# Performance work log

Measured on AMD Instinct MI355X. Metric: run time of the kernel, lower is better.

Reference implementation:

```python
import jax, jax.numpy as jnp
import numpy as np

B_, H_, W_, C_ = 8, 56, 56, 96
D_ = int(C_ * 2.0)          # d_inner = 192
N_ = 16                     # d_state
K_ = 4                      # scan directions
R_ = (C_ + 15) // 16        # dt_rank 'auto' = 6
MLP_H = 4 * C_
EPS = 1e-5


def setup_inputs() -> dict:
    key = jax.random.key(0)
    ks = jax.random.split(key, 16)
    s = 0.02
    rn = lambda k, sh, sc=1.0: jax.random.normal(k, sh, dtype=jnp.float32) * sc
    return dict(
        x=rn(ks[0], (B_, H_, W_, C_)),
        ln1_w=jnp.ones((C_,), jnp.float32), ln1_b=jnp.zeros((C_,), jnp.float32),
        in_proj_w=rn(ks[1], (2 * D_, C_), s),
        conv_w=rn(ks[2], (D_, 1, 3, 3), s), conv_b=jnp.zeros((D_,), jnp.float32),
        x_proj_w=rn(ks[3], (K_, R_ + 2 * N_, D_), s),
        dt_proj_w=rn(ks[4], (K_, D_, R_), s),
        dt_proj_b=rn(ks[5], (K_, D_), 0.1),
        A_logs=jax.random.uniform(ks[6], (K_ * D_, N_), jnp.float32, 0.0, 3.0),
        Ds=jnp.ones((K_ * D_,), jnp.float32),
        out_norm_w=jnp.ones((D_,), jnp.float32), out_norm_b=jnp.zeros((D_,), jnp.float32),
        out_proj_w=rn(ks[7], (C_, D_), s),
        ln2_w=jnp.ones((C_,), jnp.float32), ln2_b=jnp.zeros((C_,), jnp.float32),
        fc1_w=rn(ks[8], (MLP_H, C_), s), fc1_b=jnp.zeros((MLP_H,), jnp.float32),
        fc2_w=rn(ks[9], (C_, MLP_H), s), fc2_b=jnp.zeros((C_,), jnp.float32),
    )


def layer_norm(x, w, b):
    m = x.mean(-1, keepdims=True)
    v = ((x - m) ** 2).mean(-1, keepdims=True)
    return (x - m) / jnp.sqrt(v + EPS) * w + b


def ss2d(x, in_proj_w, conv_w, conv_b, x_proj_w, dt_proj_w, dt_proj_b,
         A_logs, Ds, out_norm_w, out_norm_b, out_proj_w):
    Bn, Hh, Ww, C = x.shape
    L = Hh * Ww
    xz = x @ in_proj_w.T                       # (B,H,W,2D)
    xc, z = jnp.split(xz, 2, axis=-1)
    xc = xc.transpose(0, 3, 1, 2)              # (B,D,H,W)
    xc = jax.lax.conv_general_dilated(xc, conv_w, (1, 1), 'SAME',
                                      feature_group_count=D_)
    xc = jax.nn.silu(xc + conv_b[None, :, None, None])
    # cross-scan: 4 traversal orders, each (B,D,L)
    x0 = xc.reshape(Bn, D_, L)
    x1 = xc.transpose(0, 1, 3, 2).reshape(Bn, D_, L)
    xs = jnp.stack([x0, x1, x0[..., ::-1], x1[..., ::-1]], axis=1)  # (B,K,D,L)
    xdbl = jnp.einsum('bkdl,kcd->bkcl', xs, x_proj_w)
    dts, Bs, Cs = jnp.split(xdbl, [R_, R_ + N_], axis=2)            # (B,K,R,L),(B,K,N,L)x2
    dts = jnp.einsum('bkrl,kdr->bkdl', dts, dt_proj_w)
    dts = jax.nn.softplus(dts + dt_proj_b[None, :, :, None])        # (B,K,D,L)
    A = -jnp.exp(A_logs).reshape(K_, D_, N_)                        # (K,D,N)

    def step(h, inp):
        xt, dtt, Bt, Ct = inp                  # (B,K,D),(B,K,D),(B,K,N),(B,K,N)
        h = h * jnp.exp(dtt[..., None] * A) + (dtt * xt)[..., None] * Bt[:, :, None, :]
        return h, jnp.einsum('bkdn,bkn->bkd', h, Ct)

    inps = (xs.transpose(3, 0, 1, 2), dts.transpose(3, 0, 1, 2),
            Bs.transpose(3, 0, 1, 2), Cs.transpose(3, 0, 1, 2))
    h0 = jnp.zeros((Bn, K_, D_, N_), jnp.float32)
    _, ys = jax.lax.scan(step, h0, inps)       # (L,B,K,D)
    ys = ys.transpose(1, 2, 3, 0)              # (B,K,D,L)
    ys = ys + Ds.reshape(K_, D_)[None, :, :, None] * xs
    # cross-merge: undo flips and transposed order
    y = ys[:, 0] + ys[:, 2, :, ::-1]
    y = y + (ys[:, 1] + ys[:, 3, :, ::-1]).reshape(Bn, D_, Ww, Hh) \
            .transpose(0, 1, 3, 2).reshape(Bn, D_, L)
    y = y.transpose(0, 2, 1).reshape(Bn, Hh, Ww, D_)
    y = layer_norm(y, out_norm_w, out_norm_b)
    y = y * jax.nn.silu(z)
    return y @ out_proj_w.T


def reference(x, ln1_w, ln1_b, in_proj_w, conv_w, conv_b, x_proj_w, dt_proj_w,
              dt_proj_b, A_logs, Ds, out_norm_w, out_norm_b, out_proj_w,
              ln2_w, ln2_b, fc1_w, fc1_b, fc2_w, fc2_b):
    # norm -> SS2D -> residual
    x = x + ss2d(layer_norm(x, ln1_w, ln1_b), in_proj_w, conv_w, conv_b,
                 x_proj_w, dt_proj_w, dt_proj_b, A_logs, Ds,
                 out_norm_w, out_norm_b, out_proj_w)
    # norm -> MLP -> residual
    h = layer_norm(x, ln2_w, ln2_b)
    h = jax.nn.gelu(h @ fc1_w.T + fc1_b) @ fc2_w.T + fc2_b
    return x + h
```

## Files before the change

### kernel.cpp

```cpp
#include <hip/hip_runtime.h>
#include <hip/hip_bf16.h>

typedef __hip_bfloat16 bf16;
typedef short bf16x8 __attribute__((ext_vector_type(8)));
typedef float f32x4 __attribute__((ext_vector_type(4)));

#define BBATCH 8
#define HHH 56
#define WWW 56
#define CCH 96
#define DIN 192
#define NST 16
#define KDIR 4
#define RDT 6
#define LLEN 3136
#define BLTOT 25088
#define SSEG 64
#define SEGL 49
#define PJC 38
#define PJW 152
#define PJS 40
#define PJS1 24
#define MLPH 384

#if defined(__has_builtin)
#if __has_builtin(__builtin_amdgcn_exp2f)
#define EXP2F(x) __builtin_amdgcn_exp2f(x)
#endif
#if __has_builtin(__builtin_amdgcn_logf)
#define LOG2F_(x) __builtin_amdgcn_logf(x)
#endif
#endif
#ifndef EXP2F
#define EXP2F(x) __expf((x) * 0.69314718056f)
#endif
#ifndef LOG2F_
#define LOG2F_(x) (__logf(x) * 1.44269504f)
#endif
#define LOG2E 1.44269504f

__device__ __forceinline__ float b2f(bf16 v) { return __bfloat162float(v); }
__device__ __forceinline__ bf16  f2b(float v) { return __float2bfloat16(v); }
__device__ __forceinline__ unsigned short f2bu(float f) {
    union { bf16 h; unsigned short u; } c; c.h = __float2bfloat16(f); return c.u;
}
__device__ __forceinline__ float sigm(float x) { return 1.f / (1.f + __expf(-x)); }
__device__ __forceinline__ float softplusf(float x) {
    float t = EXP2F(-fabsf(x) * LOG2E);
    return fmaxf(x, 0.f) + 0.69314718f * LOG2F_(1.f + t);
}
__device__ __forceinline__ float geluf(float v) {
    float u = 0.7978845608028654f * (v + 0.044715f * v * v * v);
    float ey = __expf(2.f * u);
    float th = 1.f - 2.f / (ey + 1.f);
    return 0.5f * v * (1.f + th);
}

__device__ __forceinline__ int pos_map(int k, int l) {
    if (k & 2) l = LLEN - 1 - l;
    if (k & 1) { int q = l / WWW; int r = l - q * WWW; return r * WWW + q; }
    return l;
}

__global__ __launch_bounds__(256) void ln_rows(
    const float* __restrict__ xin, const float* __restrict__ w,
    const float* __restrict__ b, unsigned short* __restrict__ xn) {
    int row = blockIdx.x * 4 + (threadIdx.x >> 6);
    int lane = threadIdx.x & 63;
    const float* xr = xin + (size_t)row * 96;
    float2 v = make_float2(0.f, 0.f);
    if (lane < 48) v = *(const float2*)&xr[lane * 2];
    float s = v.x + v.y, s2 = v.x * v.x + v.y * v.y;
    for (int o = 32; o; o >>= 1) {
        s += __shfl_down(s, o);
        s2 += __shfl_down(s2, o);
    }
    s = __shfl(s, 0); s2 = __shfl(s2, 0);
    float m = s * (1.f / 96.f);
    float var = s2 * (1.f / 96.f) - m * m;
    float rs = rsqrtf(var + 1e-5f);
    if (lane < 48) {
        float o0 = (v.x - m) * rs * w[lane * 2] + b[lane * 2];
        float o1 = (v.y - m) * rs * w[lane * 2 + 1] + b[lane * 2 + 1];
        ushort2 u; u.x = f2bu(o0); u.y = f2bu(o1);
        *(ushort2*)&xn[(size_t)row * 96 + lane * 2] = u;
    }
}

template<int N, int K, int EPI>
__global__ __launch_bounds__(256) void gemm_mfma(
    const unsigned short* __restrict__ X, const float* __restrict__ W,
    const float* __restrict__ bias, const float* __restrict__ res,
    void* __restrict__ out0v, void* __restrict__ out1v) {
    __shared__ unsigned short a_sh[256 * 40];
    __shared__ unsigned short b_sh[64 * 40];
    const int t = threadIdx.x;
    const int P0 = blockIdx.x * 256;
    const int N0 = blockIdx.y * 64;
    const int w = t >> 6, lane = t & 63, q = lane >> 4, nl = lane & 15;
    f32x4 acc[4][4];
#pragma unroll
    for (int i = 0; i < 4; ++i)
#pragma unroll
        for (int j = 0; j < 4; ++j)
            acc[i][j] = (f32x4){0.f, 0.f, 0.f, 0.f};
    for (int k0 = 0; k0 < K; k0 += 32) {
        __syncthreads();
#pragma unroll
        for (int it = 0; it < 4; ++it) {
            int idx = t + it * 256;
            int pr = idx >> 2, kq = idx & 3;
            uint4 v = *(const uint4*)&X[(size_t)(P0 + pr) * K + k0 + kq * 8];
            *(uint4*)&a_sh[pr * 40 + kq * 8] = v;
        }
#pragma unroll
        for (int it = 0; it < 2; ++it) {
            int idx = t + it * 256;
            int nr = idx >> 3, kq = idx & 7;
            int ng = N0 + nr; if (ng > N - 1) ng = N - 1;
            float4 v = *(const float4*)&W[(size_t)ng * K + k0 + kq * 4];
            ushort4 u;
            u.x = f2bu(v.x); u.y = f2bu(v.y); u.z = f2bu(v.z); u.w = f2bu(v.w);
            *(ushort4*)&b_sh[nr * 40 + kq * 4] = u;
        }
        __syncthreads();
        bf16x8 af[4], bfr[4];
#pragma unroll
        for (int mf = 0; mf < 4; ++mf)
            af[mf] = *(const bf16x8*)&a_sh[(w * 64 + mf * 16 + nl) * 40 + q * 8];
#pragma unroll
        for (int nf = 0; nf < 4; ++nf)
            bfr[nf] = *(const bf16x8*)&b_sh[(nf * 16 + nl) * 40 + q * 8];
#pragma unroll
        for (int mf = 0; mf < 4; ++mf)
#pragma unroll
            for (int nf = 0; nf < 4; ++nf)
                acc[mf][nf] = __builtin_amdgcn_mfma_f32_16x16x32_bf16(
                    af[mf], bfr[nf], acc[mf][nf], 0, 0, 0);
    }
#pragma unroll
    for (int mf = 0; mf < 4; ++mf) {
#pragma unroll
        for (int nf = 0; nf < 4; ++nf) {
#pragma unroll
            for (int r = 0; r < 4; ++r) {
                float v = acc[mf][nf][r];
                size_t pos = (size_t)P0 + w * 64 + mf * 16 + q * 4 + r;
                int n = N0 + nf * 16 + nl;
                if constexpr (EPI == 0) {
                    unsigned short* xc = (unsigned short*)out0v;
                    unsigned short* zz = (unsigned short*)out1v;
                    if (n < 192) xc[pos * 192 + n] = f2bu(v);
                    else         zz[pos * 192 + (n - 192)] = f2bu(v);
                } else if constexpr (EPI == 1) {
                    if (n < 152) ((float*)out0v)[pos * 152 + n] = v;
                } else if constexpr (EPI == 2) {
                    if (n < 96) ((float*)out0v)[pos * 96 + n] = res[pos * 96 + n] + v;
                } else if constexpr (EPI == 3) {
                    ((unsigned short*)out0v)[pos * 384 + n] = f2bu(geluf(v + bias[n]));
                } else {
                    if (n < 96) ((float*)out0v)[pos * 96 + n] =
                        res[pos * 96 + n] + bias[n] + v;
                }
            }
        }
    }
}

__global__ __launch_bounds__(256) void k2_conv(
    const unsigned short* __restrict__ xcpre, const float* __restrict__ cw,
    const float* __restrict__ cb, unsigned short* __restrict__ xconv) {
    int idx = blockIdx.x * 256 + threadIdx.x;
    int dd = idx % 96;
    int P = idx / 96;
    int d0 = dd * 2;
    int b = P / LLEN, l = P - b * LLEN;
    int h = l / WWW, w = l - h * WWW;
    float acc0 = cb[d0], acc1 = cb[d0 + 1];
#pragma unroll
    for (int i = 0; i < 3; ++i) {
        int hh = h + i - 1;
        if (hh < 0 || hh >= HHH) continue;
#pragma unroll
        for (int j = 0; j < 3; ++j) {
            int ww = w + j - 1;
            if (ww < 0 || ww >= WWW) continue;
            ushort2 xv = *(const ushort2*)&xcpre[
                ((size_t)(b * LLEN + hh * WWW + ww)) * DIN + d0];
            union { unsigned short u; bf16 h_; } c0, c1;
            c0.u = xv.x; c1.u = xv.y;
            acc0 = fmaf(b2f(c0.h_), cw[d0 * 9 + i * 3 + j], acc0);
            acc1 = fmaf(b2f(c1.h_), cw[(d0 + 1) * 9 + i * 3 + j], acc1);
        }
    }
    acc0 = acc0 * sigm(acc0);
    acc1 = acc1 * sigm(acc1);
    ushort2 o; o.x = f2bu(acc0); o.y = f2bu(acc1);
    *(ushort2*)&xconv[(size_t)P * DIN + d0] = o;
}

__global__ __launch_bounds__(192) void k4_scan1(
    const bf16* __restrict__ xconv, const float* __restrict__ proj,
    const float* __restrict__ dtw, const float* __restrict__ dtb,
    const float* __restrict__ Alog, float* __restrict__ hloc,
    float* __restrict__ tsum) {
    __shared__ float pl[SEGL * PJS1];
    __shared__ int posl[SEGL];
    const int bid = blockIdx.x;
    const int s = bid & 63, k = (bid >> 6) & 3, b = bid >> 8;
    const int d = threadIdx.x;
    const int l0 = s * SEGL;
    for (int q = d; q < SEGL * 22; q += 192) {
        int st = q / 22, c = q - st * 22;
        int p = pos_map(k, l0 + st);
        int ofs = (c < 6) ? c : c + 2;
        pl[st * PJS1 + ofs] = proj[(size_t)(b * LLEN + p) * PJW + k * PJC + c];
    }
    if (d < SEGL) posl[d] = pos_map(k, l0 + d) * DIN;
    float w6[RDT];
#pragma unroll
    for (int r = 0; r < RDT; ++r) w6[r] = dtw[(k * DIN + d) * RDT + r];
    const float bias = dtb[k * DIN + d];
    float a2[NST];
#pragma unroll
    for (int n = 0; n < NST; ++n)
        a2[n] = -__expf(Alog[(k * DIN + d) * NST + n]) * LOG2E;
    float h[NST];
#pragma unroll
    for (int n = 0; n < NST; ++n) h[n] = 0.f;
    float T = 0.f;
    __syncthreads();
    const bf16* xg = xconv + (size_t)b * LLEN * DIN + d;
    for (int bt = 0; bt < 7; ++bt) {
        int off7[7]; float xv7[7];
#pragma unroll
        for (int i = 0; i < 7; ++i) off7[i] = posl[bt * 7 + i];
#pragma unroll
        for (int i = 0; i < 7; ++i) xv7[i] = b2f(xg[off7[i]]);
#pragma unroll
        for (int i = 0; i < 7; ++i) {
            const float* rowf = &pl[(bt * 7 + i) * PJS1];
            float4 g0 = *(const float4*)(rowf);
            float2 g1 = *(const float2*)(rowf + 4);
            float dtv = bias;
            dtv = fmaf(g0.x, w6[0], dtv); dtv = fmaf(g0.y, w6[1], dtv);
            dtv = fmaf(g0.z, w6[2], dtv); dtv = fmaf(g0.w, w6[3], dtv);
            dtv = fmaf(g1.x, w6[4], dtv); dtv = fmaf(g1.y, w6[5], dtv);
            dtv = softplusf(dtv);
            T += dtv;
            float u = dtv * xv7[i];
#pragma unroll
            for (int g = 0; g < 4; ++g) {
                float4 Bv = *(const float4*)(rowf + 8 + 4 * g);
                float e0 = EXP2F(dtv * a2[4 * g + 0]);
                float e1 = EXP2F(dtv * a2[4 * g + 1]);
                float e2 = EXP2F(dtv * a2[4 * g + 2]);
                float e3 = EXP2F(dtv * a2[4 * g + 3]);
                h[4 * g + 0] = fmaf(h[4 * g + 0], e0, u * Bv.x);
                h[4 * g + 1] = fmaf(h[4 * g + 1], e1, u * Bv.y);
                h[4 * g + 2] = fmaf(h[4 * g + 2], e2, u * Bv.z);
                h[4 * g + 3] = fmaf(h[4 * g + 3], e3, u * Bv.w);
            }
        }
    }
    size_t base = ((size_t)bid * DIN + d) * NST;
#pragma unroll
    for (int n = 0; n < NST; ++n) hloc[base + n] = h[n];
    tsum[bid * DIN + d] = T;
}

__global__ __launch_bounds__(256) void k5_carry(
    const float* hloc, const float* __restrict__ tsum,
    const float* __restrict__ Alog, float* hin) {
    int g = blockIdx.x * 256 + threadIdx.x;
    int n = g & 15;
    int dk = g >> 4;
    int d = dk % DIN;
    int bk = dk / DIN;
    int k = bk & 3;
    float a2 = -__expf(Alog[(k * DIN + d) * NST + n]) * LOG2E;
    float Hc = 0.f;
    for (int s = 0; s < SSEG; ++s) {
        int bid = bk * SSEG + s;
        size_t idx = ((size_t)bid * DIN + d) * NST + n;
        float hl = hloc[idx];
        float Tv = tsum[bid * DIN + d];
        hin[idx] = Hc;
        Hc = fmaf(EXP2F(a2 * Tv), Hc, hl);
    }
}

__global__ __launch_bounds__(192) void k6_scan2(
    const bf16* __restrict__ xconv, const float* __restrict__ proj,
    const float* __restrict__ dtw, const float* __restrict__ dtb,
    const float* __restrict__ Alog, const float* __restrict__ Dsp,
    const float* __restrict__ hin, bf16* __restrict__ ysm) {
    __shared__ float pl[SEGL * PJS];
    __shared__ int posl[SEGL];
    const int bid = blockIdx.x;
    const int s = bid & 63, k = (bid >> 6) & 3, b = bid >> 8;
    const int d = threadIdx.x;
    const int l0 = s * SEGL;
    for (int q = d; q < SEGL * PJC; q += 192) {
        int st = q / PJC, c = q - st * PJC;
        int p = pos_map(k, l0 + st);
        int ofs = (c < 6) ? c : c + 2;
        pl[st * PJS + ofs] = proj[(size_t)(b * LLEN + p) * PJW + k * PJC + c];
    }
    if (d < SEGL) posl[d] = pos_map(k, l0 + d) * DIN;
    float w6[RDT];
#pragma unroll
    for (int r = 0; r < RDT; ++r) w6[r] = dtw[(k * DIN + d) * RDT + r];
    const float bias = dtb[k * DIN + d];
    const float dsv = Dsp[k * DIN + d];
    float a2[NST];
#pragma unroll
    for (int n = 0; n < NST; ++n)
        a2[n] = -__expf(Alog[(k * DIN + d) * NST + n]) * LOG2E;
    float h[NST];
    size_t hbase = ((size_t)bid * DIN + d) * NST;
#pragma unroll
    for (int n = 0; n < NST; ++n) h[n] = hin[hbase + n];
    __syncthreads();
    const bf16* xg = xconv + (size_t)b * LLEN * DIN + d;
    bf16* ysg = ysm + ((size_t)(b * KDIR + k) * LLEN) * DIN + d;
    for (int bt = 0; bt < 7; ++bt) {
        int off7[7]; float xv7[7];
#pragma unroll
        for (int i = 0; i < 7; ++i) off7[i] = posl[bt * 7 + i];
#pragma unroll
        for (int i = 0; i < 7; ++i) xv7[i] = b2f(xg[off7[i]]);
#pragma unroll
        for (int i = 0; i < 7; ++i) {
            const float* rowf = &pl[(bt * 7 + i) * PJS];
            float4 g0 = *(const float4*)(rowf);
            float2 g1 = *(const float2*)(rowf + 4);
            float dtv = bias;
            dtv = fmaf(g0.x, w6[0], dtv); dtv = fmaf(g0.y, w6[1], dtv);
            dtv = fmaf(g0.z, w6[2], dtv); dtv = fmaf(g0.w, w6[3], dtv);
            dtv = fmaf(g1.x, w6[4], dtv); dtv = fmaf(g1.y, w6[5], dtv);
            dtv = softplusf(dtv);
            float u = dtv * xv7[i];
            float y = dsv * xv7[i];
#pragma unroll
            for (int g = 0; g < 4; ++g) {
                float4 Bv = *(const float4*)(rowf + 8 + 4 * g);
                float4 Cv = *(const float4*)(rowf + 24 + 4 * g);
                float e0 = EXP2F(dtv * a2[4 * g + 0]);
                float e1 = EXP2F(dtv * a2[4 * g + 1]);
                float e2 = EXP2F(dtv * a2[4 * g + 2]);
                float e3 = EXP2F(dtv * a2[4 * g + 3]);
                h[4 * g + 0] = fmaf(h[4 * g + 0], e0, u * Bv.x);
                h[4 * g + 1] = fmaf(h[4 * g + 1], e1, u * Bv.y);
                h[4 * g + 2] = fmaf(h[4 * g + 2], e2, u * Bv.z);
                h[4 * g + 3] = fmaf(h[4 * g + 3], e3, u * Bv.w);
                y = fmaf(h[4 * g + 0], Cv.x, y);
                y = fmaf(h[4 * g + 1], Cv.y, y);
                y = fmaf(h[4 * g + 2], Cv.z, y);
                y = fmaf(h[4 * g + 3], Cv.w, y);
            }
            ysg[off7[i]] = f2b(y);
        }
    }
}

__global__ __launch_bounds__(256) void k65_merge(
    const bf16* __restrict__ ysm, const bf16* __restrict__ z,
    const float* __restrict__ onw, const float* __restrict__ onb,
    bf16* __restrict__ ymod) {
    __shared__ float rb[16 * DIN];
    __shared__ float ps[256], pq[256];
    __shared__ float mrow[16], srow[16];
    const int t = threadIdx.x;
    const int P0 = blockIdx.x * 16;
    for (int q = t; q < 16 * DIN; q += 256) {
        int pos = q / DIN, c = q - pos * DIN;
        int P = P0 + pos;
        int b = P / LLEN, l = P - b * LLEN;
        size_t base = ((size_t)(b * KDIR) * LLEN + l) * DIN + c;
        size_t pstr = (size_t)LLEN * DIN;
        float v = b2f(ysm[base]) + b2f(ysm[base + pstr]) +
                  b2f(ysm[base + 2 * pstr]) + b2f(ysm[base + 3 * pstr]);
        rb[q] = v;
    }
    __syncthreads();
    {
        int pos = t >> 4, part = t & 15;
        float s = 0.f, s2 = 0.f;
        for (int i = 0; i < 12; ++i) {
            float v = rb[pos * DIN + part * 12 + i];
            s += v; s2 += v * v;
        }
        ps[pos * 16 + part] = s; pq[pos * 16 + part] = s2;
    }
    __syncthreads();
    if (t < 16) {
        float s = 0.f, s2 = 0.f;
        for (int i = 0; i < 16; ++i) { s += ps[t * 16 + i]; s2 += pq[t * 16 + i]; }
        float m = s * (1.f / DIN);
        float v = s2 * (1.f / DIN) - m * m;
        mrow[t] = m; srow[t] = rsqrtf(v + 1e-5f);
    }
    __syncthreads();
    for (int q = t; q < 16 * DIN; q += 256) {
        int pos = q / DIN, c = q - pos * DIN;
        int P = P0 + pos;
        float v = (rb[q] - mrow[pos]) * srow[pos] * onw[c] + onb[c];
        float zv = b2f(z[(size_t)P * DIN + c]);
        v *= zv * sigm(zv);
        ymod[(size_t)P * DIN + c] = f2b(v);
    }
}

extern "C" void kernel_launch(void* const* d_in, const int* in_sizes, int n_in,
                              void* d_out, int out_size, void* d_ws, size_t ws_size,
                              hipStream_t stream) {
    const float* x      = (const float*)d_in[0];
    const float* ln1w   = (const float*)d_in[1];
    const float* ln1b   = (const float*)d_in[2];
    const float* inpW   = (const float*)d_in[3];
    const float* convW  = (const float*)d_in[4];
    const float* convB  = (const float*)d_in[5];
    const float* xprojW = (const float*)d_in[6];
    const float* dtW    = (const float*)d_in[7];
    const float* dtB    = (const float*)d_in[8];
    const float* Alog   = (const float*)d_in[9];
    const float* Dsp    = (const float*)d_in[10];
    const float* onw    = (const float*)d_in[11];
    const float* onb    = (const float*)d_in[12];
    const float* outW   = (const float*)d_in[13];
    const float* ln2w   = (const float*)d_in[14];
    const float* ln2b   = (const float*)d_in[15];
    const float* fc1W   = (const float*)d_in[16];
    const float* fc1b   = (const float*)d_in[17];
    const float* fc2W   = (const float*)d_in[18];
    const float* fc2b   = (const float*)d_in[19];
    float* out = (float*)d_out;

    char* ws = (char*)d_ws;
    unsigned short* z_us    = (unsigned short*)(ws + 0);
    bf16*  z_bf             = (bf16*)z_us;
    bf16*  xconv_bf         = (bf16*)(ws + 9633792);
    float* proj_f           = (float*)(ws + 19267584);
    bf16*  ymod_bf          = (bf16*)(ws + 19267584);
    unsigned short* xn_us   = (unsigned short*)(ws + 34521088);
    float* tsum_f           = (float*)(ws + 34521088);
    unsigned short* xcpre_us= (unsigned short*)(ws + 39337984);
    float* hloc_f           = (float*)(ws + 48971776);
    float* hin_f            = hloc_f;
    float* y1_f             = (float*)(ws + 48971776);
    unsigned short* y1n_us  = (unsigned short*)(ws + 58605568);
    bf16*  ysm_bf           = (bf16*)(ws + 74137600);
    unsigned short* hmlp_us = (unsigned short*)(ws + 74137600);

    ln_rows<<<6272, 256, 0, stream>>>(x, ln1w, ln1b, xn_us);
    gemm_mfma<384, 96, 0><<<dim3(98, 6), 256, 0, stream>>>(
        xn_us, inpW, nullptr, nullptr, xcpre_us, z_us);
    k2_conv<<<9408, 256, 0, stream>>>(xcpre_us, convW, convB,
                                      (unsigned short*)xconv_bf);
    gemm_mfma<152, 192, 1><<<dim3(98, 3), 256, 0, stream>>>(
        (const unsigned short*)xconv_bf, xprojW, nullptr, nullptr, proj_f, nullptr);
    k4_scan1<<<2048, 192, 0, stream>>>(xconv_bf, proj_f, dtW, dtB, Alog, hloc_f, tsum_f);
    k5_carry<<<384, 256, 0, stream>>>(hloc_f, tsum_f, Alog, hin_f);
    k6_scan2<<<2048, 192, 0, stream>>>(xconv_bf, proj_f, dtW, dtB, Alog, Dsp, hin_f, ysm_bf);
    k65_merge<<<1568, 256, 0, stream>>>(ysm_bf, z_bf, onw, onb, ymod_bf);
    gemm_mfma<96, 192, 2><<<dim3(98, 2), 256, 0, stream>>>(
        (const unsigned short*)ymod_bf, outW, nullptr, x, y1_f, nullptr);
    ln_rows<<<6272, 256, 0, stream>>>(y1_f, ln2w, ln2b, y1n_us);
    gemm_mfma<384, 96, 3><<<dim3(98, 6), 256, 0, stream>>>(
        y1n_us, fc1W, fc1b, nullptr, hmlp_us, nullptr);
    gemm_mfma<96, 384, 4><<<dim3(98, 2), 256, 0, stream>>>(
        hmlp_us, fc2W, fc2b, y1_f, out, nullptr);
}
```

Baseline: 396.6 us.

## Halve GEMM row tile, widen conv vectors, pack scan math into v_pk_f32

GEMM blocks now cover 128 rows instead of 256, which doubles the grid for better CU occupancy on the small GEMMs. The depthwise conv now handles 4 channels per thread with 8-byte loads, halving its grid. Both scan kernels keep the state and decay terms in float2 pairs and use inline-asm v_pk_mul_f32 and v_pk_fma_f32 to cut VALU instruction count in the recurrence. The y reduction in scan2 is split into two packed partial sums, which changes the summation order slightly. The inline asm may also block some compiler scheduling.

```diff
diff --git a/kernel.cpp b/kernel.cpp
--- a/kernel.cpp
+++ b/kernel.cpp
@@ -39,10 +39,24 @@
 #endif
 #define LOG2E 1.44269504f
 
+__device__ __forceinline__ float2 pk_mul(float2 a, float2 b) {
+    float2 d;
+    asm("v_pk_mul_f32 %0, %1, %2" : "=v"(d) : "v"(a), "v"(b));
+    return d;
+}
+__device__ __forceinline__ float2 pk_fma(float2 a, float2 b, float2 c) {
+    float2 d;
+    asm("v_pk_fma_f32 %0, %1, %2, %3" : "=v"(d) : "v"(a), "v"(b), "v"(c));
+    return d;
+}
+
 __device__ __forceinline__ float b2f(bf16 v) { return __bfloat162float(v); }
 __device__ __forceinline__ bf16  f2b(float v) { return __float2bfloat16(v); }
 __device__ __forceinline__ unsigned short f2bu(float f) {
     union { bf16 h; unsigned short u; } c; c.h = __float2bfloat16(f); return c.u;
+}
+__device__ __forceinline__ float bu2f(unsigned short u) {
+    union { unsigned short u; bf16 h; } c; c.u = u; return __bfloat162float(c.h);
 }
 __device__ __forceinline__ float sigm(float x) { return 1.f / (1.f + __expf(-x)); }
 __device__ __forceinline__ float softplusf(float x) {
@@ -92,22 +106,22 @@
     const unsigned short* __restrict__ X, const float* __restrict__ W,
     const float* __restrict__ bias, const float* __restrict__ res,
     void* __restrict__ out0v, void* __restrict__ out1v) {
-    __shared__ unsigned short a_sh[256 * 40];
+    __shared__ unsigned short a_sh[128 * 40];
     __shared__ unsigned short b_sh[64 * 40];
     const int t = threadIdx.x;
-    const int P0 = blockIdx.x * 256;
+    const int P0 = blockIdx.x * 128;
     const int N0 = blockIdx.y * 64;
     const int w = t >> 6, lane = t & 63, q = lane >> 4, nl = lane & 15;
-    f32x4 acc[4][4];
-#pragma unroll
-    for (int i = 0; i < 4; ++i)
+    f32x4 acc[2][4];
+#pragma unroll
+    for (int i = 0; i < 2; ++i)
 #pragma unroll
         for (int j = 0; j < 4; ++j)
             acc[i][j] = (f32x4){0.f, 0.f, 0.f, 0.f};
     for (int k0 = 0; k0 < K; k0 += 32) {
         __syncthreads();
 #pragma unroll
-        for (int it = 0; it < 4; ++it) {
+        for (int it = 0; it < 2; ++it) {
             int idx = t + it * 256;
             int pr = idx >> 2, kq = idx & 3;
             uint4 v = *(const uint4*)&X[(size_t)(P0 + pr) * K + k0 + kq * 8];
@@ -124,28 +138,28 @@
             *(ushort4*)&b_sh[nr * 40 + kq * 4] = u;
         }
         __syncthreads();
-        bf16x8 af[4], bfr[4];
-#pragma unroll
-        for (int mf = 0; mf < 4; ++mf)
-            af[mf] = *(const bf16x8*)&a_sh[(w * 64 + mf * 16 + nl) * 40 + q * 8];
+        bf16x8 af[2], bfr[4];
+#pragma unroll
+        for (int mf = 0; mf < 2; ++mf)
+            af[mf] = *(const bf16x8*)&a_sh[(w * 32 + mf * 16 + nl) * 40 + q * 8];
 #pragma unroll
         for (int nf = 0; nf < 4; ++nf)
             bfr[nf] = *(const bf16x8*)&b_sh[(nf * 16 + nl) * 40 + q * 8];
 #pragma unroll
-        for (int mf = 0; mf < 4; ++mf)
+        for (int mf = 0; mf < 2; ++mf)
 #pragma unroll
             for (int nf = 0; nf < 4; ++nf)
                 acc[mf][nf] = __builtin_amdgcn_mfma_f32_16x16x32_bf16(
                     af[mf], bfr[nf], acc[mf][nf], 0, 0, 0);
     }
 #pragma unroll
-    for (int mf = 0; mf < 4; ++mf) {
+    for (int mf = 0; mf < 2; ++mf) {
 #pragma unroll
         for (int nf = 0; nf < 4; ++nf) {
 #pragma unroll
             for (int r = 0; r < 4; ++r) {
                 float v = acc[mf][nf][r];
-                size_t pos = (size_t)P0 + w * 64 + mf * 16 + q * 4 + r;
+                size_t pos = (size_t)P0 + w * 32 + mf * 16 + q * 4 + r;
                 int n = N0 + nf * 16 + nl;
                 if constexpr (EPI == 0) {
                     unsigned short* xc = (unsigned short*)out0v;
@@ -171,12 +185,12 @@
     const unsigned short* __restrict__ xcpre, const float* __restrict__ cw,
     const float* __restrict__ cb, unsigned short* __restrict__ xconv) {
     int idx = blockIdx.x * 256 + threadIdx.x;
-    int dd = idx % 96;
-    int P = idx / 96;
-    int d0 = dd * 2;
+    int dd = idx % 48;
+    int P = idx / 48;
+    int d0 = dd * 4;
     int b = P / LLEN, l = P - b * LLEN;
     int h = l / WWW, w = l - h * WWW;
-    float acc0 = cb[d0], acc1 = cb[d0 + 1];
+    float acc0 = cb[d0], acc1 = cb[d0 + 1], acc2 = cb[d0 + 2], acc3 = cb[d0 + 3];
 #pragma unroll
     for (int i = 0; i < 3; ++i) {
         int hh = h + i - 1;
@@ -185,18 +199,19 @@
         for (int j = 0; j < 3; ++j) {
             int ww = w + j - 1;
             if (ww < 0 || ww >= WWW) continue;
-            ushort2 xv = *(const ushort2*)&xcpre[
+            ushort4 xv = *(const ushort4*)&xcpre[
                 ((size_t)(b * LLEN + hh * WWW + ww)) * DIN + d0];
-            union { unsigned short u; bf16 h_; } c0, c1;
-            c0.u = xv.x; c1.u = xv.y;
-            acc0 = fmaf(b2f(c0.h_), cw[d0 * 9 + i * 3 + j], acc0);
-            acc1 = fmaf(b2f(c1.h_), cw[(d0 + 1) * 9 + i * 3 + j], acc1);
-        }
-    }
-    acc0 = acc0 * sigm(acc0);
-    acc1 = acc1 * sigm(acc1);
-    ushort2 o; o.x = f2bu(acc0); o.y = f2bu(acc1);
-    *(ushort2*)&xconv[(size_t)P * DIN + d0] = o;
+            acc0 = fmaf(bu2f(xv.x), cw[(d0 + 0) * 9 + i * 3 + j], acc0);
+            acc1 = fmaf(bu2f(xv.y), cw[(d0 + 1) * 9 + i * 3 + j], acc1);
+            acc2 = fmaf(bu2f(xv.z), cw[(d0 + 2) * 9 + i * 3 + j], acc2);
+            acc3 = fmaf(bu2f(xv.w), cw[(d0 + 3) * 9 + i * 3 + j], acc3);
+        }
+    }
+    acc0 = acc0 * sigm(acc0); acc1 = acc1 * sigm(acc1);
+    acc2 = acc2 * sigm(acc2); acc3 = acc3 * sigm(acc3);
+    ushort4 o;
+    o.x = f2bu(acc0); o.y = f2bu(acc1); o.z = f2bu(acc2); o.w = f2bu(acc3);
+    *(ushort4*)&xconv[(size_t)P * DIN + d0] = o;
 }
 
 __global__ __launch_bounds__(192) void k4_scan1(
@@ -221,13 +236,15 @@
 #pragma unroll
     for (int r = 0; r < RDT; ++r) w6[r] = dtw[(k * DIN + d) * RDT + r];
     const float bias = dtb[k * DIN + d];
-    float a2[NST];
-#pragma unroll
-    for (int n = 0; n < NST; ++n)
-        a2[n] = -__expf(Alog[(k * DIN + d) * NST + n]) * LOG2E;
-    float h[NST];
-#pragma unroll
-    for (int n = 0; n < NST; ++n) h[n] = 0.f;
+    float2 a2[8];
+#pragma unroll
+    for (int j = 0; j < 8; ++j) {
+        a2[j].x = -__expf(Alog[(k * DIN + d) * NST + 2 * j]) * LOG2E;
+        a2[j].y = -__expf(Alog[(k * DIN + d) * NST + 2 * j + 1]) * LOG2E;
+    }
+    float2 h2[8];
+#pragma unroll
+    for (int j = 0; j < 8; ++j) h2[j] = make_float2(0.f, 0.f);
     float T = 0.f;
     __syncthreads();
     const bf16* xg = xconv + (size_t)b * LLEN * DIN + d;
@@ -248,24 +265,26 @@
             dtv = fmaf(g1.x, w6[4], dtv); dtv = fmaf(g1.y, w6[5], dtv);
             dtv = softplusf(dtv);
             T += dtv;
-            float u = dtv * xv7[i];
+            float2 dt2 = make_float2(dtv, dtv);
+            float2 u2 = make_float2(dtv * xv7[i], dtv * xv7[i]);
 #pragma unroll
             for (int g = 0; g < 4; ++g) {
                 float4 Bv = *(const float4*)(rowf + 8 + 4 * g);
-                float e0 = EXP2F(dtv * a2[4 * g + 0]);
-                float e1 = EXP2F(dtv * a2[4 * g + 1]);
-                float e2 = EXP2F(dtv * a2[4 * g + 2]);
-                float e3 = EXP2F(dtv * a2[4 * g + 3]);
-                h[4 * g + 0] = fmaf(h[4 * g + 0], e0, u * Bv.x);
-                h[4 * g + 1] = fmaf(h[4 * g + 1], e1, u * Bv.y);
-                h[4 * g + 2] = fmaf(h[4 * g + 2], e2, u * Bv.z);
-                h[4 * g + 3] = fmaf(h[4 * g + 3], e3, u * Bv.w);
+                float2 Blo = make_float2(Bv.x, Bv.y);
+                float2 Bhi = make_float2(Bv.z, Bv.w);
+                float2 alo = pk_mul(dt2, a2[2 * g]);
+                float2 ahi = pk_mul(dt2, a2[2 * g + 1]);
+                float2 elo, ehi;
+                elo.x = EXP2F(alo.x); elo.y = EXP2F(alo.y);
+                ehi.x = EXP2F(ahi.x); ehi.y = EXP2F(ahi.y);
+                h2[2 * g]     = pk_fma(h2[2 * g],     elo, pk_mul(u2, Blo));
+                h2[2 * g + 1] = pk_fma(h2[2 * g + 1], ehi, pk_mul(u2, Bhi));
             }
         }
     }
     size_t base = ((size_t)bid * DIN + d) * NST;
 #pragma unroll
-    for (int n = 0; n < NST; ++n) hloc[base + n] = h[n];
+    for (int j = 0; j < 8; ++j) *(float2*)&hloc[base + 2 * j] = h2[j];
     tsum[bid * DIN + d] = T;
 }
 
@@ -313,14 +332,16 @@
     for (int r = 0; r < RDT; ++r) w6[r] = dtw[(k * DIN + d) * RDT + r];
     const float bias = dtb[k * DIN + d];
     const float dsv = Dsp[k * DIN + d];
-    float a2[NST];
-#pragma unroll
-    for (int n = 0; n < NST; ++n)
-        a2[n] = -__expf(Alog[(k * DIN + d) * NST + n]) * LOG2E;
-    float h[NST];
+    float2 a2[8];
+#pragma unroll
+    for (int j = 0; j < 8; ++j) {
+        a2[j].x = -__expf(Alog[(k * DIN + d) * NST + 2 * j]) * LOG2E;
+        a2[j].y = -__expf(Alog[(k * DIN + d) * NST + 2 * j + 1]) * LOG2E;
+    }
+    float2 h2[8];
     size_t hbase = ((size_t)bid * DIN + d) * NST;
 #pragma unroll
-    for (int n = 0; n < NST; ++n) h[n] = hin[hbase + n];
+    for (int j = 0; j < 8; ++j) h2[j] = *(const float2*)&hin[hbase + 2 * j];
     __syncthreads();
     const bf16* xg = xconv + (size_t)b * LLEN * DIN + d;
     bf16* ysg = ysm + ((size_t)(b * KDIR + k) * LLEN) * DIN + d;
@@ -340,26 +361,29 @@
             dtv = fmaf(g0.z, w6[2], dtv); dtv = fmaf(g0.w, w6[3], dtv);
             dtv = fmaf(g1.x, w6[4], dtv); dtv = fmaf(g1.y, w6[5], dtv);
             dtv = softplusf(dtv);
-            float u = dtv * xv7[i];
-            float y = dsv * xv7[i];
+            float2 dt2 = make_float2(dtv, dtv);
+            float2 u2 = make_float2(dtv * xv7[i], dtv * xv7[i]);
+            float2 yac0 = make_float2(0.f, 0.f), yac1 = make_float2(0.f, 0.f);
 #pragma unroll
             for (int g = 0; g < 4; ++g) {
                 float4 Bv = *(const float4*)(rowf + 8 + 4 * g);
                 float4 Cv = *(const float4*)(rowf + 24 + 4 * g);
-                float e0 = EXP2F(dtv * a2[4 * g + 0]);
-                float e1 = EXP2F(dtv * a2[4 * g + 1]);
-                float e2 = EXP2F(dtv * a2[4 * g + 2]);
-                float e3 = EXP2F(dtv * a2[4 * g + 3]);
-                h[4 * g + 0] = fmaf(h[4 * g + 0], e0, u * Bv.x);
-                h[4 * g + 1] = fmaf(h[4 * g + 1], e1, u * Bv.y);
-                h[4 * g + 2] = fmaf(h[4 * g + 2], e2, u * Bv.z);
-                h[4 * g + 3] = fmaf(h[4 * g + 3], e3, u * Bv.w);
-                y = fmaf(h[4 * g + 0], Cv.x, y);
-                y = fmaf(h[4 * g + 1], Cv.y, y);
-                y = fmaf(h[4 * g + 2], Cv.z, y);
-                y = fmaf(h[4 * g + 3], Cv.w, y);
+                float2 Blo = make_float2(Bv.x, Bv.y);
+                float2 Bhi = make_float2(Bv.z, Bv.w);
+                float2 Clo = make_float2(Cv.x, Cv.y);
+                float2 Chi = make_float2(Cv.z, Cv.w);
+                float2 alo = pk_mul(dt2, a2[2 * g]);
+                float2 ahi = pk_mul(dt2, a2[2 * g + 1]);
+                float2 elo, ehi;
+                elo.x = EXP2F(alo.x); elo.y = EXP2F(alo.y);
+                ehi.x = EXP2F(ahi.x); ehi.y = EXP2F(ahi.y);
+                h2[2 * g]     = pk_fma(h2[2 * g],     elo, pk_mul(u2, Blo));
+                h2[2 * g + 1] = pk_fma(h2[2 * g + 1], ehi, pk_mul(u2, Bhi));
+                yac0 = pk_fma(h2[2 * g],     Clo, yac0);
+                yac1 = pk_fma(h2[2 * g + 1], Chi, yac1);
             }
-            ysg[off7[i]] = f2b(y);
+            float y = (yac0.x + yac0.y) + (yac1.x + yac1.y);
+            ysg[off7[i]] = f2b(fmaf(dsv, xv7[i], y));
         }
     }
 }
@@ -454,21 +478,21 @@
     unsigned short* hmlp_us = (unsigned short*)(ws + 74137600);
 
     ln_rows<<<6272, 256, 0, stream>>>(x, ln1w, ln1b, xn_us);
-    gemm_mfma<384, 96, 0><<<dim3(98, 6), 256, 0, stream>>>(
+    gemm_mfma<384, 96, 0><<<dim3(196, 6), 256, 0, stream>>>(
         xn_us, inpW, nullptr, nullptr, xcpre_us, z_us);
-    k2_conv<<<9408, 256, 0, stream>>>(xcpre_us, convW, convB,
+    k2_conv<<<4704, 256, 0, stream>>>(xcpre_us, convW, convB,
                                       (unsigned short*)xconv_bf);
-    gemm_mfma<152, 192, 1><<<dim3(98, 3), 256, 0, stream>>>(
+    gemm_mfma<152, 192, 1><<<dim3(196, 3), 256, 0, stream>>>(
         (const unsigned short*)xconv_bf, xprojW, nullptr, nullptr, proj_f, nullptr);
     k4_scan1<<<2048, 192, 0, stream>>>(xconv_bf, proj_f, dtW, dtB, Alog, hloc_f, tsum_f);
     k5_carry<<<384, 256, 0, stream>>>(hloc_f, tsum_f, Alog, hin_f);
     k6_scan2<<<2048, 192, 0, stream>>>(xconv_bf, proj_f, dtW, dtB, Alog, Dsp, hin_f, ysm_bf);
     k65_merge<<<1568, 256, 0, stream>>>(ysm_bf, z_bf, onw, onb, ymod_bf);
-    gemm_mfma<96, 192, 2><<<dim3(98, 2), 256, 0, stream>>>(
+    gemm_mfma<96, 192, 2><<<dim3(196, 2), 256, 0, stream>>>(
         (const unsigned short*)ymod_bf, outW, nullptr, x, y1_f, nullptr);
     ln_rows<<<6272, 256, 0, stream>>>(y1_f, ln2w, ln2b, y1n_us);
-    gemm_mfma<384, 96, 3><<<dim3(98, 6), 256, 0, stream>>>(
+    gemm_mfma<384, 96, 3><<<dim3(196, 6), 256, 0, stream>>>(
         y1n_us, fc1W, fc1b, nullptr, hmlp_us, nullptr);
-    gemm_mfma<96, 384, 4><<<dim3(98, 2), 256, 0, stream>>>(
+    gemm_mfma<96, 384, 4><<<dim3(196, 2), 256, 0, stream>>>(
         hmlp_us, fc2W, fc2b, y1_f, out, nullptr);
 }
```

New measurement: 387.2 us. 1.02x faster.
